# Kernel optimization log

Hardware: AMD Instinct MI355X
Metric: run time of the kernel (lower is better)

## Reference

```python
import jax, jax.numpy as jnp
import numpy as np

B, S, D, H = 2, 2048, 1024, 16
DH = D // H
MASKED_BIAS = -10000.0


def setup_inputs() -> dict:
    key = jax.random.key(0)
    k1, k2, k3 = jax.random.split(key, 3)
    x = jax.random.normal(k1, (B, S, D), dtype=jnp.float32)
    w_attn = jax.random.normal(k2, (D, 3 * D), dtype=jnp.float32) * 0.02
    b_attn = jnp.zeros((3 * D,), dtype=jnp.float32)
    w_proj = jax.random.normal(k3, (D, D), dtype=jnp.float32) * 0.02
    b_proj = jnp.zeros((D,), dtype=jnp.float32)
    return {"x": x, "w_attn": w_attn, "b_attn": b_attn, "w_proj": w_proj, "b_proj": b_proj}


def reference(x, w_attn, b_attn, w_proj, b_proj):
    # c_attn (Conv1D): [B,S,D] @ [D,3D] + b -> [B,S,3D]
    qkv = x @ w_attn + b_attn
    q, k, v = jnp.split(qkv, 3, axis=-1)

    def split_heads(t):  # [B,S,D] -> [B,H,S,DH]
        return t.reshape(B, S, H, DH).transpose(0, 2, 1, 3)

    q, k, v = split_heads(q), split_heads(k), split_heads(v)

    # scores: [B,H,S,S], scaled by sqrt(head_dim) (value.size(-1))
    scores = jnp.einsum('bhqd,bhkd->bhqk', q, k) / jnp.float32(np.sqrt(DH))

    # causal mask via torch.where against masked_bias (-10000.0), not -inf
    causal = jnp.tril(jnp.ones((S, S), dtype=bool))
    scores = jnp.where(causal, scores, jnp.float32(MASKED_BIAS))

    attn = jax.nn.softmax(scores, axis=-1)  # attn_pdrop = 0 -> dropout is identity
    ctx = jnp.einsum('bhqk,bhkd->bhqd', attn, v)  # [B,H,S,DH]

    # merge heads -> [B,S,D], then c_proj (resid_pdrop = 0)
    ctx = ctx.transpose(0, 2, 1, 3).reshape(B, S, D)
    out = ctx @ w_proj + b_proj
    return out
```

## Files before the change

### kernel.cpp

```cpp
#include <hip/hip_runtime.h>
#include <hip/hip_bf16.h>


#define BB 2
#define SS 2048
#define DD 1024
#define HH 16
#define DHH 64
#define MTOK (BB * SS)
#define N3D (3 * DD)

typedef __attribute__((ext_vector_type(8))) short bf16x8;
typedef __attribute__((ext_vector_type(4))) float f32x4;
typedef __attribute__((ext_vector_type(4))) short short4v;

__device__ __forceinline__ short f2bf(float f) {
  unsigned int x = __float_as_uint(f);
  unsigned int r = (x + 0x7fffu + ((x >> 16) & 1u)) >> 16;
  return (short)r;
}

__device__ __forceinline__ unsigned int cvtpk_bf16(float lo, float hi) {
  unsigned int r;
  asm("v_cvt_pk_bf16_f32 %0, %1, %2" : "=v"(r) : "v"(lo), "v"(hi));
  return r;
}

__global__ void cast_bf16_k(const float* __restrict__ in, short* __restrict__ out, int n4) {
  int i = blockIdx.x * blockDim.x + threadIdx.x;
  if (i < n4) {
    float4 v = reinterpret_cast<const float4*>(in)[i];
    short4v o;
    o[0] = f2bf(v.x); o[1] = f2bf(v.y); o[2] = f2bf(v.z); o[3] = f2bf(v.w);
    reinterpret_cast<short4v*>(out)[i] = o;
  }
}

__global__ void transpose_cast_k(const float* __restrict__ W, short* __restrict__ Wt, int K, int N) {
  __shared__ float t[32][33];
  int n0 = blockIdx.x * 32, k0 = blockIdx.y * 32;
  int tx = threadIdx.x, ty = threadIdx.y;
#pragma unroll
  for (int i = 0; i < 4; ++i)
    t[ty + 8 * i][tx] = W[(size_t)(k0 + ty + 8 * i) * N + n0 + tx];
  __syncthreads();
#pragma unroll
  for (int i = 0; i < 4; ++i)
    Wt[(size_t)(n0 + ty + 8 * i) * K + k0 + tx] = f2bf(t[tx][ty + 8 * i]);
}

__global__ void extract_vt_k(const short* __restrict__ qkv, short* __restrict__ vt) {
  __shared__ short t[32][33];
  int s0 = blockIdx.x * 32, d0 = blockIdx.y * 32;
  int bh = blockIdx.z;
  int b = bh >> 4, h = bh & 15;
  int tx = threadIdx.x, ty = threadIdx.y;
#pragma unroll
  for (int i = 0; i < 4; ++i)
    t[ty + 8 * i][tx] =
        qkv[(size_t)(b * SS + s0 + ty + 8 * i) * N3D + 2 * DD + h * DHH + d0 + tx];
  __syncthreads();
#pragma unroll
  for (int i = 0; i < 4; ++i)
    vt[(size_t)(bh * DHH + d0 + ty + 8 * i) * SS + s0 + tx] = t[tx][ty + 8 * i];
}

template <int OUTF32>
__global__ __launch_bounds__(256) void gemm128_k(const short* __restrict__ A,
                                                 const short* __restrict__ Bt,
                                                 const float* __restrict__ bias,
                                                 void* __restrict__ Cout,
                                                 int M, int N, int K) {
  __shared__ short As[128 * 64];
  __shared__ short Bs[128 * 64];
  int tid = threadIdx.x;
  int m0 = blockIdx.y * 128, n0 = blockIdx.x * 128;
  int w = tid >> 6, lane = tid & 63;
  int wr = w >> 1, wc = w & 1;
  int ln16 = lane & 15, l16 = lane >> 4;

  f32x4 acc[4][4] = {};

  int lrow0 = w * 32 + (lane >> 3);
  int blk_p = lane & 7;

  for (int k0 = 0; k0 < K; k0 += 64) {
#pragma unroll
    for (int i = 0; i < 4; ++i) {
      int row_p = lrow0 + i * 8;
      int colE = ((blk_p ^ (row_p & 7)) << 3);
      __builtin_amdgcn_global_load_lds(
          (const __attribute__((address_space(1))) unsigned int*)&A[(size_t)(m0 + row_p) * K + k0 + colE],
          (__attribute__((address_space(3))) unsigned int*)&As[(w * 4 + i) * 512],
          16, 0, 0);
      __builtin_amdgcn_global_load_lds(
          (const __attribute__((address_space(1))) unsigned int*)&Bt[(size_t)(n0 + row_p) * K + k0 + colE],
          (__attribute__((address_space(3))) unsigned int*)&Bs[(w * 4 + i) * 512],
          16, 0, 0);
    }
    __syncthreads();
#pragma unroll
    for (int kk = 0; kk < 2; ++kk) {
      bf16x8 a[4], bfr[4];
#pragma unroll
      for (int mi = 0; mi < 4; ++mi) {
        int row = wr * 64 + mi * 16 + ln16;
        int blk = (kk * 4 + l16) ^ (row & 7);
        a[mi] = *reinterpret_cast<const bf16x8*>(&As[row * 64 + blk * 8]);
      }
#pragma unroll
      for (int ni = 0; ni < 4; ++ni) {
        int row = wc * 64 + ni * 16 + ln16;
        int blk = (kk * 4 + l16) ^ (row & 7);
        bfr[ni] = *reinterpret_cast<const bf16x8*>(&Bs[row * 64 + blk * 8]);
      }
#pragma unroll
      for (int mi = 0; mi < 4; ++mi)
#pragma unroll
        for (int ni = 0; ni < 4; ++ni)
          acc[mi][ni] = __builtin_amdgcn_mfma_f32_16x16x32_bf16(a[mi], bfr[ni], acc[mi][ni], 0, 0, 0);
    }
    __syncthreads();
  }

#pragma unroll
  for (int mi = 0; mi < 4; ++mi)
#pragma unroll
    for (int ni = 0; ni < 4; ++ni)
#pragma unroll
      for (int ri = 0; ri < 4; ++ri) {
        int row = m0 + wr * 64 + mi * 16 + l16 * 4 + ri;
        int col = n0 + wc * 64 + ni * 16 + ln16;
        float v = acc[mi][ni][ri] + bias[col];
        if (OUTF32) {
          reinterpret_cast<float*>(Cout)[(size_t)row * N + col] = v;
        } else {
          if (col < DD) v *= 0.125f;
          reinterpret_cast<short*>(Cout)[(size_t)row * N + col] = f2bf(v);
        }
      }
}

#define MASKV -3.0e38f
__global__ __launch_bounds__(512) void flash_attn_k(const short* __restrict__ qkv,
                                                    const short* __restrict__ vt,
                                                    short* __restrict__ ctx) {
  __shared__ __align__(16) char smem[53248];
  short (*Ks)[64][72] = reinterpret_cast<short(*)[64][72]>(smem);
  short (*Vs)[64][72] = reinterpret_cast<short(*)[64][72]>(smem + 18432);
  short* Psr = reinterpret_cast<short*>(smem + 36864);
  float* Od = reinterpret_cast<float*>(smem);
  float* mls = reinterpret_cast<float*>(smem + 17408);

  int tid = threadIdx.x;
  int pj = blockIdx.x;
  int bh = blockIdx.y;
  int b = bh >> 4, h = bh & 15;
  int wg = tid >> 6, lane = tid & 63;
  int g = wg >> 2, wq = wg & 3;
  int ln16 = lane & 15, l16 = lane >> 4;
  int t8 = tid & 255;
  int tb = tid >> 8;
  int r0 = t8 >> 3, cc0 = (t8 & 7) << 3;
  int psq = (wg << 10) + (ln16 << 6);

  const short* kbase = qkv + (size_t)(b * SS) * N3D + DD + h * DHH;
  const short* vbase = vt + (size_t)(bh * DHH) * SS;

#pragma unroll 1
  for (int ti = 0; ti < 2; ++ti) {
    int qt = ti ? pj : 31 - pj;
    int q0 = qt * 64;

    bf16x8 qf[2];
    {
      const short* qrow = qkv + (size_t)(b * SS + q0 + wq * 16 + ln16) * N3D + h * DHH;
      qf[0] = *reinterpret_cast<const bf16x8*>(qrow + l16 * 8);
      qf[1] = *reinterpret_cast<const bf16x8*>(qrow + 32 + l16 * 8);
    }
    float m_ = -1e30f, l_ = 0.f;
    f32x4 cacc[4] = {};

    int ns = (qt + 2) >> 1;
    uint4 kr0, kr1, vr0, vr1;
    {
      int kt_s = tb <= qt ? tb : qt;
      kr0 = *reinterpret_cast<const uint4*>(kbase + (size_t)(kt_s * 64 + r0) * N3D + cc0);
      kr1 = *reinterpret_cast<const uint4*>(kbase + (size_t)(kt_s * 64 + r0 + 32) * N3D + cc0);
      vr0 = *reinterpret_cast<const uint4*>(vbase + (size_t)r0 * SS + kt_s * 64 + cc0);
      vr1 = *reinterpret_cast<const uint4*>(vbase + (size_t)(r0 + 32) * SS + kt_s * 64 + cc0);
    }

#pragma unroll 1
    for (int s = 0; s < ns; ++s) {
      *reinterpret_cast<uint4*>(&Ks[tb][r0][cc0]) = kr0;
      *reinterpret_cast<uint4*>(&Ks[tb][r0 + 32][cc0]) = kr1;
      *reinterpret_cast<uint4*>(&Vs[tb][r0][cc0]) = vr0;
      *reinterpret_cast<uint4*>(&Vs[tb][r0 + 32][cc0]) = vr1;
      __syncthreads();

      {
        int kt_n = 2 * (s + 1) + tb;
        if (kt_n > qt) kt_n = qt;
        kr0 = *reinterpret_cast<const uint4*>(kbase + (size_t)(kt_n * 64 + r0) * N3D + cc0);
        kr1 = *reinterpret_cast<const uint4*>(kbase + (size_t)(kt_n * 64 + r0 + 32) * N3D + cc0);
        vr0 = *reinterpret_cast<const uint4*>(vbase + (size_t)r0 * SS + kt_n * 64 + cc0);
        vr1 = *reinterpret_cast<const uint4*>(vbase + (size_t)(r0 + 32) * SS + kt_n * 64 + cc0);
      }

      int kt_c = 2 * s + g;
      if (kt_c <= qt) {
        f32x4 sacc[4] = {};
#pragma unroll
        for (int kk = 0; kk < 2; ++kk)
#pragma unroll
          for (int ni = 0; ni < 4; ++ni) {
            bf16x8 kf = *reinterpret_cast<const bf16x8*>(&Ks[g][ni * 16 + ln16][kk * 32 + l16 * 8]);
            sacc[ni] = __builtin_amdgcn_mfma_f32_16x16x32_bf16(kf, qf[kk], sacc[ni], 0, 0, 0);
          }

        float p[4][4];
        float mx = MASKV;
        if (kt_c == qt) {
          int qg = q0 + wq * 16 + ln16;
#pragma unroll
          for (int ni = 0; ni < 4; ++ni)
#pragma unroll
            for (int ri = 0; ri < 4; ++ri) {
              int kg = kt_c * 64 + ni * 16 + l16 * 4 + ri;
              float v = (kg > qg) ? MASKV : sacc[ni][ri];
              p[ni][ri] = v;
              mx = fmaxf(mx, v);
            }
        } else {
#pragma unroll
          for (int ni = 0; ni < 4; ++ni)
#pragma unroll
            for (int ri = 0; ri < 4; ++ri) {
              p[ni][ri] = sacc[ni][ri];
              mx = fmaxf(mx, sacc[ni][ri]);
            }
        }
        mx = fmaxf(mx, __shfl_xor(mx, 16));
        mx = fmaxf(mx, __shfl_xor(mx, 32));

        int keep = __all(mx <= m_ + 8.0f);
        float mn = m_;
        if (!keep) {
          mn = fmaxf(m_, mx);
          float sc = __expf(m_ - mn);
          l_ *= sc;
          float scr[4];
#pragma unroll
          for (int ri = 0; ri < 4; ++ri) scr[ri] = __shfl(sc, l16 * 4 + ri);
#pragma unroll
          for (int di = 0; di < 4; ++di)
#pragma unroll
            for (int ri = 0; ri < 4; ++ri) cacc[di][ri] *= scr[ri];
          m_ = mn;
        }

        float sum = 0.f;
#pragma unroll
        for (int ni = 0; ni < 4; ++ni)
#pragma unroll
          for (int ri = 0; ri < 4; ++ri) {
            float e = __expf(p[ni][ri] - mn);
            p[ni][ri] = e;
            sum += e;
          }
        sum += __shfl_xor(sum, 16);
        sum += __shfl_xor(sum, 32);
        l_ += sum;

#pragma unroll
        for (int ni = 0; ni < 4; ++ni) {
          uint2 u;
          u.x = cvtpk_bf16(p[ni][0], p[ni][1]);
          u.y = cvtpk_bf16(p[ni][2], p[ni][3]);
          int idx = psq + ((((ni << 1) + (l16 >> 1)) ^ (ln16 & 7)) << 3) + ((l16 & 1) << 2);
          *reinterpret_cast<uint2*>(&Psr[idx]) = u;
        }
        asm volatile("s_waitcnt lgkmcnt(0)" ::: "memory");

#pragma unroll
        for (int kk = 0; kk < 2; ++kk) {
          bf16x8 pa = *reinterpret_cast<const bf16x8*>(
              &Psr[psq + ((((kk << 2) + l16) ^ (ln16 & 7)) << 3)]);
#pragma unroll
          for (int di = 0; di < 4; ++di) {
            bf16x8 vb = *reinterpret_cast<const bf16x8*>(&Vs[g][di * 16 + ln16][kk * 32 + l16 * 8]);
            cacc[di] = __builtin_amdgcn_mfma_f32_16x16x32_bf16(pa, vb, cacc[di], 0, 0, 0);
          }
        }
      }
      __syncthreads();
    }

    if (g == 1) {
      if (l16 == 0) { mls[wq * 16 + ln16] = m_; mls[64 + wq * 16 + ln16] = l_; }
#pragma unroll
      for (int di = 0; di < 4; ++di)
#pragma unroll
        for (int ri = 0; ri < 4; ++ri)
          Od[wq * 1040 + (l16 * 4 + ri) * 65 + di * 16 + ln16] = cacc[di][ri];
    }
    __syncthreads();
    if (g == 0) {
      float m1 = mls[wq * 16 + ln16], l1 = mls[64 + wq * 16 + ln16];
      float mM = fmaxf(m_, m1);
      float e0 = __expf(m_ - mM), e1 = __expf(m1 - mM);
      float inv = 1.f / (l_ * e0 + l1 * e1);
      float e0r[4], e1r[4], ivr[4];
#pragma unroll
      for (int ri = 0; ri < 4; ++ri) {
        int src = l16 * 4 + ri;
        e0r[ri] = __shfl(e0, src);
        e1r[ri] = __shfl(e1, src);
        ivr[ri] = __shfl(inv, src);
      }
#pragma unroll
      for (int di = 0; di < 4; ++di)
#pragma unroll
        for (int ri = 0; ri < 4; ++ri) {
          float a1 = Od[wq * 1040 + (l16 * 4 + ri) * 65 + di * 16 + ln16];
          float o = (cacc[di][ri] * e0r[ri] + a1 * e1r[ri]) * ivr[ri];
          int row = q0 + wq * 16 + l16 * 4 + ri;
          int col = h * DHH + di * 16 + ln16;
          ctx[(size_t)(b * SS + row) * DD + col] = f2bf(o);
        }
    }
    __syncthreads();
  }
}

extern "C" void kernel_launch(void* const* d_in, const int* in_sizes, int n_in,
                              void* d_out, int out_size, void* d_ws, size_t ws_size,
                              hipStream_t stream) {
  const float* x      = (const float*)d_in[0];
  const float* w_attn = (const float*)d_in[1];
  const float* b_attn = (const float*)d_in[2];
  const float* w_proj = (const float*)d_in[3];
  const float* b_proj = (const float*)d_in[4];
  float* out = (float*)d_out;

  char* ws = (char*)d_ws;
  short* xb     = (short*)(ws);
  short* wattnT = (short*)(ws + 8388608);
  short* wprojT = (short*)(ws + 14680064);
  short* qkv    = (short*)(ws + 16777216);
  short* vt     = (short*)(ws + 41943040);
  short* ctx    = (short*)(ws + 50331648);

  {
    int n4 = (MTOK * DD) / 4;
    cast_bf16_k<<<(n4 + 255) / 256, 256, 0, stream>>>(x, xb, n4);
  }
  transpose_cast_k<<<dim3(N3D / 32, DD / 32), dim3(32, 8), 0, stream>>>(w_attn, wattnT, DD, N3D);
  transpose_cast_k<<<dim3(DD / 32, DD / 32), dim3(32, 8), 0, stream>>>(w_proj, wprojT, DD, DD);
  gemm128_k<0><<<dim3(N3D / 128, MTOK / 128), 256, 0, stream>>>(xb, wattnT, b_attn, qkv, MTOK, N3D, DD);
  extract_vt_k<<<dim3(SS / 32, DHH / 32, BB * HH), dim3(32, 8), 0, stream>>>(qkv, vt);
  flash_attn_k<<<dim3(16, BB * HH), 512, 0, stream>>>(qkv, vt, ctx);
  gemm128_k<1><<<dim3(DD / 128, MTOK / 128), 256, 0, stream>>>(ctx, wprojT, b_proj, out, MTOK, DD, DD);
}
```

Measured before the change: 127.3 us.

## Launch one query tile per block and XOR-swizzle K/V shared memory

Result: slower. 144.7 us (+13.6%).

```diff
diff --git a/kernel.cpp b/kernel.cpp
--- a/kernel.cpp
+++ b/kernel.cpp
@@ -145,192 +145,189 @@
 __global__ __launch_bounds__(512) void flash_attn_k(const short* __restrict__ qkv,
                                                     const short* __restrict__ vt,
                                                     short* __restrict__ ctx) {
-  __shared__ __align__(16) char smem[53248];
-  short (*Ks)[64][72] = reinterpret_cast<short(*)[64][72]>(smem);
-  short (*Vs)[64][72] = reinterpret_cast<short(*)[64][72]>(smem + 18432);
-  short* Psr = reinterpret_cast<short*>(smem + 36864);
+  __shared__ __align__(16) char smem[49152];
+  short* Sm = reinterpret_cast<short*>(smem);
   float* Od = reinterpret_cast<float*>(smem);
   float* mls = reinterpret_cast<float*>(smem + 17408);
 
   int tid = threadIdx.x;
-  int pj = blockIdx.x;
+  int qt = 31 - blockIdx.x;
   int bh = blockIdx.y;
   int b = bh >> 4, h = bh & 15;
+  int q0 = qt * 64;
   int wg = tid >> 6, lane = tid & 63;
   int g = wg >> 2, wq = wg & 3;
   int ln16 = lane & 15, l16 = lane >> 4;
   int t8 = tid & 255;
   int tb = tid >> 8;
-  int r0 = t8 >> 3, cc0 = (t8 & 7) << 3;
-  int psq = (wg << 10) + (ln16 << 6);
+  int r0 = t8 >> 3, cb = t8 & 7;
+  int ksw = tb * 4096 + r0 * 64 + ((cb ^ (r0 & 7)) << 3);
+  int psq = 16384 + (wg << 10) + (ln16 << 6);
 
   const short* kbase = qkv + (size_t)(b * SS) * N3D + DD + h * DHH;
   const short* vbase = vt + (size_t)(bh * DHH) * SS;
 
+  bf16x8 qf[2];
+  {
+    const short* qrow = qkv + (size_t)(b * SS + q0 + wq * 16 + ln16) * N3D + h * DHH;
+    qf[0] = *reinterpret_cast<const bf16x8*>(qrow + l16 * 8);
+    qf[1] = *reinterpret_cast<const bf16x8*>(qrow + 32 + l16 * 8);
+  }
+  float m_ = -1e30f, l_ = 0.f;
+  f32x4 cacc[4] = {};
+
+  int ns = (qt + 2) >> 1;
+  uint4 kr0, kr1, vr0, vr1;
+  {
+    int kt_s = tb <= qt ? tb : qt;
+    kr0 = *reinterpret_cast<const uint4*>(kbase + (size_t)(kt_s * 64 + r0) * N3D + cb * 8);
+    kr1 = *reinterpret_cast<const uint4*>(kbase + (size_t)(kt_s * 64 + r0 + 32) * N3D + cb * 8);
+    vr0 = *reinterpret_cast<const uint4*>(vbase + (size_t)r0 * SS + kt_s * 64 + cb * 8);
+    vr1 = *reinterpret_cast<const uint4*>(vbase + (size_t)(r0 + 32) * SS + kt_s * 64 + cb * 8);
+  }
+
 #pragma unroll 1
-  for (int ti = 0; ti < 2; ++ti) {
-    int qt = ti ? pj : 31 - pj;
-    int q0 = qt * 64;
-
-    bf16x8 qf[2];
+  for (int s = 0; s < ns; ++s) {
+    *reinterpret_cast<uint4*>(&Sm[ksw]) = kr0;
+    *reinterpret_cast<uint4*>(&Sm[ksw + 2048]) = kr1;
+    *reinterpret_cast<uint4*>(&Sm[8192 + ksw]) = vr0;
+    *reinterpret_cast<uint4*>(&Sm[8192 + ksw + 2048]) = vr1;
+    __syncthreads();
+
     {
-      const short* qrow = qkv + (size_t)(b * SS + q0 + wq * 16 + ln16) * N3D + h * DHH;
-      qf[0] = *reinterpret_cast<const bf16x8*>(qrow + l16 * 8);
-      qf[1] = *reinterpret_cast<const bf16x8*>(qrow + 32 + l16 * 8);
-    }
-    float m_ = -1e30f, l_ = 0.f;
-    f32x4 cacc[4] = {};
-
-    int ns = (qt + 2) >> 1;
-    uint4 kr0, kr1, vr0, vr1;
-    {
-      int kt_s = tb <= qt ? tb : qt;
-      kr0 = *reinterpret_cast<const uint4*>(kbase + (size_t)(kt_s * 64 + r0) * N3D + cc0);
-      kr1 = *reinterpret_cast<const uint4*>(kbase + (size_t)(kt_s * 64 + r0 + 32) * N3D + cc0);
-      vr0 = *reinterpret_cast<const uint4*>(vbase + (size_t)r0 * SS + kt_s * 64 + cc0);
-      vr1 = *reinterpret_cast<const uint4*>(vbase + (size_t)(r0 + 32) * SS + kt_s * 64 + cc0);
-    }
-
-#pragma unroll 1
-    for (int s = 0; s < ns; ++s) {
-      *reinterpret_cast<uint4*>(&Ks[tb][r0][cc0]) = kr0;
-      *reinterpret_cast<uint4*>(&Ks[tb][r0 + 32][cc0]) = kr1;
-      *reinterpret_cast<uint4*>(&Vs[tb][r0][cc0]) = vr0;
-      *reinterpret_cast<uint4*>(&Vs[tb][r0 + 32][cc0]) = vr1;
-      __syncthreads();
-
-      {
-        int kt_n = 2 * (s + 1) + tb;
-        if (kt_n > qt) kt_n = qt;
-        kr0 = *reinterpret_cast<const uint4*>(kbase + (size_t)(kt_n * 64 + r0) * N3D + cc0);
-        kr1 = *reinterpret_cast<const uint4*>(kbase + (size_t)(kt_n * 64 + r0 + 32) * N3D + cc0);
-        vr0 = *reinterpret_cast<const uint4*>(vbase + (size_t)r0 * SS + kt_n * 64 + cc0);
-        vr1 = *reinterpret_cast<const uint4*>(vbase + (size_t)(r0 + 32) * SS + kt_n * 64 + cc0);
-      }
-
-      int kt_c = 2 * s + g;
-      if (kt_c <= qt) {
-        f32x4 sacc[4] = {};
-#pragma unroll
-        for (int kk = 0; kk < 2; ++kk)
-#pragma unroll
-          for (int ni = 0; ni < 4; ++ni) {
-            bf16x8 kf = *reinterpret_cast<const bf16x8*>(&Ks[g][ni * 16 + ln16][kk * 32 + l16 * 8]);
-            sacc[ni] = __builtin_amdgcn_mfma_f32_16x16x32_bf16(kf, qf[kk], sacc[ni], 0, 0, 0);
+      int kt_n = 2 * (s + 1) + tb;
+      if (kt_n > qt) kt_n = qt;
+      kr0 = *reinterpret_cast<const uint4*>(kbase + (size_t)(kt_n * 64 + r0) * N3D + cb * 8);
+      kr1 = *reinterpret_cast<const uint4*>(kbase + (size_t)(kt_n * 64 + r0 + 32) * N3D + cb * 8);
+      vr0 = *reinterpret_cast<const uint4*>(vbase + (size_t)r0 * SS + kt_n * 64 + cb * 8);
+      vr1 = *reinterpret_cast<const uint4*>(vbase + (size_t)(r0 + 32) * SS + kt_n * 64 + cb * 8);
+    }
+
+    int kt_c = 2 * s + g;
+    if (kt_c <= qt) {
+      f32x4 sacc[4] = {};
+#pragma unroll
+      for (int kk = 0; kk < 2; ++kk)
+#pragma unroll
+        for (int ni = 0; ni < 4; ++ni) {
+          int row = ni * 16 + ln16;
+          bf16x8 kf = *reinterpret_cast<const bf16x8*>(
+              &Sm[g * 4096 + row * 64 + (((kk * 4 + l16) ^ (row & 7)) << 3)]);
+          sacc[ni] = __builtin_amdgcn_mfma_f32_16x16x32_bf16(kf, qf[kk], sacc[ni], 0, 0, 0);
+        }
+
+      float p[4][4];
+      float mx = MASKV;
+      if (kt_c == qt) {
+        int qg = q0 + wq * 16 + ln16;
+#pragma unroll
+        for (int ni = 0; ni < 4; ++ni)
+#pragma unroll
+          for (int ri = 0; ri < 4; ++ri) {
+            int kg = kt_c * 64 + ni * 16 + l16 * 4 + ri;
+            float v = (kg > qg) ? MASKV : sacc[ni][ri];
+            p[ni][ri] = v;
+            mx = fmaxf(mx, v);
           }
-
-        float p[4][4];
-        float mx = MASKV;
-        if (kt_c == qt) {
-          int qg = q0 + wq * 16 + ln16;
-#pragma unroll
-          for (int ni = 0; ni < 4; ++ni)
-#pragma unroll
-            for (int ri = 0; ri < 4; ++ri) {
-              int kg = kt_c * 64 + ni * 16 + l16 * 4 + ri;
-              float v = (kg > qg) ? MASKV : sacc[ni][ri];
-              p[ni][ri] = v;
-              mx = fmaxf(mx, v);
-            }
-        } else {
-#pragma unroll
-          for (int ni = 0; ni < 4; ++ni)
-#pragma unroll
-            for (int ri = 0; ri < 4; ++ri) {
-              p[ni][ri] = sacc[ni][ri];
-              mx = fmaxf(mx, sacc[ni][ri]);
-            }
+      } else {
+#pragma unroll
+        for (int ni = 0; ni < 4; ++ni)
+#pragma unroll
+          for (int ri = 0; ri < 4; ++ri) {
+            p[ni][ri] = sacc[ni][ri];
+            mx = fmaxf(mx, sacc[ni][ri]);
+          }
+      }
+      mx = fmaxf(mx, __shfl_xor(mx, 16));
+      mx = fmaxf(mx, __shfl_xor(mx, 32));
+
+      int keep = __all(mx <= m_ + 8.0f);
+      float mn = m_;
+      if (!keep) {
+        mn = fmaxf(m_, mx);
+        float sc = __expf(m_ - mn);
+        l_ *= sc;
+        float scr[4];
+#pragma unroll
+        for (int ri = 0; ri < 4; ++ri) scr[ri] = __shfl(sc, l16 * 4 + ri);
+#pragma unroll
+        for (int di = 0; di < 4; ++di)
+#pragma unroll
+          for (int ri = 0; ri < 4; ++ri) cacc[di][ri] *= scr[ri];
+        m_ = mn;
+      }
+
+      float sum = 0.f;
+#pragma unroll
+      for (int ni = 0; ni < 4; ++ni)
+#pragma unroll
+        for (int ri = 0; ri < 4; ++ri) {
+          float e = __expf(p[ni][ri] - mn);
+          p[ni][ri] = e;
+          sum += e;
         }
-        mx = fmaxf(mx, __shfl_xor(mx, 16));
-        mx = fmaxf(mx, __shfl_xor(mx, 32));
-
-        int keep = __all(mx <= m_ + 8.0f);
-        float mn = m_;
-        if (!keep) {
-          mn = fmaxf(m_, mx);
-          float sc = __expf(m_ - mn);
-          l_ *= sc;
-          float scr[4];
-#pragma unroll
-          for (int ri = 0; ri < 4; ++ri) scr[ri] = __shfl(sc, l16 * 4 + ri);
-#pragma unroll
-          for (int di = 0; di < 4; ++di)
-#pragma unroll
-            for (int ri = 0; ri < 4; ++ri) cacc[di][ri] *= scr[ri];
-          m_ = mn;
+      sum += __shfl_xor(sum, 16);
+      sum += __shfl_xor(sum, 32);
+      l_ += sum;
+
+#pragma unroll
+      for (int ni = 0; ni < 4; ++ni) {
+        uint2 u;
+        u.x = cvtpk_bf16(p[ni][0], p[ni][1]);
+        u.y = cvtpk_bf16(p[ni][2], p[ni][3]);
+        int idx = psq + ((((ni << 1) + (l16 >> 1)) ^ (ln16 & 7)) << 3) + ((l16 & 1) << 2);
+        *reinterpret_cast<uint2*>(&Sm[idx]) = u;
+      }
+      asm volatile("s_waitcnt lgkmcnt(0)" ::: "memory");
+
+#pragma unroll
+      for (int kk = 0; kk < 2; ++kk) {
+        bf16x8 pa = *reinterpret_cast<const bf16x8*>(
+            &Sm[psq + ((((kk << 2) + l16) ^ (ln16 & 7)) << 3)]);
+#pragma unroll
+        for (int di = 0; di < 4; ++di) {
+          int row = di * 16 + ln16;
+          bf16x8 vb = *reinterpret_cast<const bf16x8*>(
+              &Sm[8192 + g * 4096 + row * 64 + (((kk * 4 + l16) ^ (row & 7)) << 3)]);
+          cacc[di] = __builtin_amdgcn_mfma_f32_16x16x32_bf16(pa, vb, cacc[di], 0, 0, 0);
         }
-
-        float sum = 0.f;
-#pragma unroll
-        for (int ni = 0; ni < 4; ++ni)
-#pragma unroll
-          for (int ri = 0; ri < 4; ++ri) {
-            float e = __expf(p[ni][ri] - mn);
-            p[ni][ri] = e;
-            sum += e;
-          }
-        sum += __shfl_xor(sum, 16);
-        sum += __shfl_xor(sum, 32);
-        l_ += sum;
-
-#pragma unroll
-        for (int ni = 0; ni < 4; ++ni) {
-          uint2 u;
-          u.x = cvtpk_bf16(p[ni][0], p[ni][1]);
-          u.y = cvtpk_bf16(p[ni][2], p[ni][3]);
-          int idx = psq + ((((ni << 1) + (l16 >> 1)) ^ (ln16 & 7)) << 3) + ((l16 & 1) << 2);
-          *reinterpret_cast<uint2*>(&Psr[idx]) = u;
-        }
-        asm volatile("s_waitcnt lgkmcnt(0)" ::: "memory");
-
-#pragma unroll
-        for (int kk = 0; kk < 2; ++kk) {
-          bf16x8 pa = *reinterpret_cast<const bf16x8*>(
-              &Psr[psq + ((((kk << 2) + l16) ^ (ln16 & 7)) << 3)]);
-#pragma unroll
-          for (int di = 0; di < 4; ++di) {
-            bf16x8 vb = *reinterpret_cast<const bf16x8*>(&Vs[g][di * 16 + ln16][kk * 32 + l16 * 8]);
-            cacc[di] = __builtin_amdgcn_mfma_f32_16x16x32_bf16(pa, vb, cacc[di], 0, 0, 0);
-          }
-        }
-      }
-      __syncthreads();
-    }
-
-    if (g == 1) {
-      if (l16 == 0) { mls[wq * 16 + ln16] = m_; mls[64 + wq * 16 + ln16] = l_; }
-#pragma unroll
-      for (int di = 0; di < 4; ++di)
-#pragma unroll
-        for (int ri = 0; ri < 4; ++ri)
-          Od[wq * 1040 + (l16 * 4 + ri) * 65 + di * 16 + ln16] = cacc[di][ri];
+      }
     }
     __syncthreads();
-    if (g == 0) {
-      float m1 = mls[wq * 16 + ln16], l1 = mls[64 + wq * 16 + ln16];
-      float mM = fmaxf(m_, m1);
-      float e0 = __expf(m_ - mM), e1 = __expf(m1 - mM);
-      float inv = 1.f / (l_ * e0 + l1 * e1);
-      float e0r[4], e1r[4], ivr[4];
+  }
+
+  if (g == 1) {
+    if (l16 == 0) { mls[wq * 16 + ln16] = m_; mls[64 + wq * 16 + ln16] = l_; }
+#pragma unroll
+    for (int di = 0; di < 4; ++di)
+#pragma unroll
+      for (int ri = 0; ri < 4; ++ri)
+        Od[wq * 1040 + (l16 * 4 + ri) * 65 + di * 16 + ln16] = cacc[di][ri];
+  }
+  __syncthreads();
+  if (g == 0) {
+    float m1 = mls[wq * 16 + ln16], l1 = mls[64 + wq * 16 + ln16];
+    float mM = fmaxf(m_, m1);
+    float e0 = __expf(m_ - mM), e1 = __expf(m1 - mM);
+    float inv = 1.f / (l_ * e0 + l1 * e1);
+    float e0r[4], e1r[4], ivr[4];
+#pragma unroll
+    for (int ri = 0; ri < 4; ++ri) {
+      int src = l16 * 4 + ri;
+      e0r[ri] = __shfl(e0, src);
+      e1r[ri] = __shfl(e1, src);
+      ivr[ri] = __shfl(inv, src);
+    }
+#pragma unroll
+    for (int di = 0; di < 4; ++di)
 #pragma unroll
       for (int ri = 0; ri < 4; ++ri) {
-        int src = l16 * 4 + ri;
-        e0r[ri] = __shfl(e0, src);
-        e1r[ri] = __shfl(e1, src);
-        ivr[ri] = __shfl(inv, src);
-      }
-#pragma unroll
-      for (int di = 0; di < 4; ++di)
-#pragma unroll
-        for (int ri = 0; ri < 4; ++ri) {
-          float a1 = Od[wq * 1040 + (l16 * 4 + ri) * 65 + di * 16 + ln16];
-          float o = (cacc[di][ri] * e0r[ri] + a1 * e1r[ri]) * ivr[ri];
-          int row = q0 + wq * 16 + l16 * 4 + ri;
-          int col = h * DHH + di * 16 + ln16;
-          ctx[(size_t)(b * SS + row) * DD + col] = f2bf(o);
-        }
-    }
-    __syncthreads();
+        float a1 = Od[wq * 1040 + (l16 * 4 + ri) * 65 + di * 16 + ln16];
+        float o = (cacc[di][ri] * e0r[ri] + a1 * e1r[ri]) * ivr[ri];
+        int row = q0 + wq * 16 + l16 * 4 + ri;
+        int col = h * DHH + di * 16 + ln16;
+        ctx[(size_t)(b * SS + row) * DD + col] = f2bf(o);
+      }
   }
 }
 
@@ -360,6 +357,6 @@
   transpose_cast_k<<<dim3(DD / 32, DD / 32), dim3(32, 8), 0, stream>>>(w_proj, wprojT, DD, DD);
   gemm128_k<0><<<dim3(N3D / 128, MTOK / 128), 256, 0, stream>>>(xb, wattnT, b_attn, qkv, MTOK, N3D, DD);
   extract_vt_k<<<dim3(SS / 32, DHH / 32, BB * HH), dim3(32, 8), 0, stream>>>(qkv, vt);
-  flash_attn_k<<<dim3(16, BB * HH), 512, 0, stream>>>(qkv, vt, ctx);
+  flash_attn_k<<<dim3(32, BB * HH), 512, 0, stream>>>(qkv, vt, ctx);
   gemm128_k<1><<<dim3(DD / 128, MTOK / 128), 256, 0, stream>>>(ctx, wprojT, b_proj, out, MTOK, DD, DD);
 }
```

## Fuse V-transpose into QKV GEMM epilogue and switch softmax to exp2

Applied to the files above, without the earlier changes.

After: 128.4 us. Within noise of the previous version (+0.8%).

```diff
diff --git a/kernel.cpp b/kernel.cpp
--- a/kernel.cpp
+++ b/kernel.cpp
@@ -9,6 +9,7 @@
 #define DHH 64
 #define MTOK (BB * SS)
 #define N3D (3 * DD)
+#define QSCALE 0.18033688f
 
 typedef __attribute__((ext_vector_type(8))) short bf16x8;
 typedef __attribute__((ext_vector_type(4))) float f32x4;
@@ -49,27 +50,12 @@
     Wt[(size_t)(n0 + ty + 8 * i) * K + k0 + tx] = f2bf(t[tx][ty + 8 * i]);
 }
 
-__global__ void extract_vt_k(const short* __restrict__ qkv, short* __restrict__ vt) {
-  __shared__ short t[32][33];
-  int s0 = blockIdx.x * 32, d0 = blockIdx.y * 32;
-  int bh = blockIdx.z;
-  int b = bh >> 4, h = bh & 15;
-  int tx = threadIdx.x, ty = threadIdx.y;
-#pragma unroll
-  for (int i = 0; i < 4; ++i)
-    t[ty + 8 * i][tx] =
-        qkv[(size_t)(b * SS + s0 + ty + 8 * i) * N3D + 2 * DD + h * DHH + d0 + tx];
-  __syncthreads();
-#pragma unroll
-  for (int i = 0; i < 4; ++i)
-    vt[(size_t)(bh * DHH + d0 + ty + 8 * i) * SS + s0 + tx] = t[tx][ty + 8 * i];
-}
-
 template <int OUTF32>
 __global__ __launch_bounds__(256) void gemm128_k(const short* __restrict__ A,
                                                  const short* __restrict__ Bt,
                                                  const float* __restrict__ bias,
                                                  void* __restrict__ Cout,
+                                                 short* __restrict__ vtout,
                                                  int M, int N, int K) {
   __shared__ short As[128 * 64];
   __shared__ short Bs[128 * 64];
@@ -135,8 +121,14 @@
         if (OUTF32) {
           reinterpret_cast<float*>(Cout)[(size_t)row * N + col] = v;
         } else {
-          if (col < DD) v *= 0.125f;
-          reinterpret_cast<short*>(Cout)[(size_t)row * N + col] = f2bf(v);
+          if (n0 < DD) v *= QSCALE;
+          short bv = f2bf(v);
+          if (n0 >= 2 * DD) {
+            int bb = row >> 11, s = row & 2047;
+            vtout[(size_t)(bb * 1024 + col - 2 * DD) * SS + s] = bv;
+          } else {
+            reinterpret_cast<short*>(Cout)[(size_t)row * N + col] = bv;
+          }
         }
       }
 }
@@ -244,11 +236,11 @@
         mx = fmaxf(mx, __shfl_xor(mx, 16));
         mx = fmaxf(mx, __shfl_xor(mx, 32));
 
-        int keep = __all(mx <= m_ + 8.0f);
+        int keep = __all(mx <= m_ + 11.5f);
         float mn = m_;
         if (!keep) {
           mn = fmaxf(m_, mx);
-          float sc = __expf(m_ - mn);
+          float sc = exp2f(m_ - mn);
           l_ *= sc;
           float scr[4];
 #pragma unroll
@@ -265,7 +257,7 @@
         for (int ni = 0; ni < 4; ++ni)
 #pragma unroll
           for (int ri = 0; ri < 4; ++ri) {
-            float e = __expf(p[ni][ri] - mn);
+            float e = exp2f(p[ni][ri] - mn);
             p[ni][ri] = e;
             sum += e;
           }
@@ -309,7 +301,7 @@
     if (g == 0) {
       float m1 = mls[wq * 16 + ln16], l1 = mls[64 + wq * 16 + ln16];
       float mM = fmaxf(m_, m1);
-      float e0 = __expf(m_ - mM), e1 = __expf(m1 - mM);
+      float e0 = exp2f(m_ - mM), e1 = exp2f(m1 - mM);
       float inv = 1.f / (l_ * e0 + l1 * e1);
       float e0r[4], e1r[4], ivr[4];
 #pragma unroll
@@ -358,8 +350,7 @@
   }
   transpose_cast_k<<<dim3(N3D / 32, DD / 32), dim3(32, 8), 0, stream>>>(w_attn, wattnT, DD, N3D);
   transpose_cast_k<<<dim3(DD / 32, DD / 32), dim3(32, 8), 0, stream>>>(w_proj, wprojT, DD, DD);
-  gemm128_k<0><<<dim3(N3D / 128, MTOK / 128), 256, 0, stream>>>(xb, wattnT, b_attn, qkv, MTOK, N3D, DD);
-  extract_vt_k<<<dim3(SS / 32, DHH / 32, BB * HH), dim3(32, 8), 0, stream>>>(qkv, vt);
+  gemm128_k<0><<<dim3(N3D / 128, MTOK / 128), 256, 0, stream>>>(xb, wattnT, b_attn, qkv, vt, MTOK, N3D, DD);
   flash_attn_k<<<dim3(16, BB * HH), 512, 0, stream>>>(qkv, vt, ctx);
-  gemm128_k<1><<<dim3(DD / 128, MTOK / 128), 256, 0, stream>>>(ctx, wprojT, b_proj, out, MTOK, DD, DD);
-}
+  gemm128_k<1><<<dim3(DD / 128, MTOK / 128), 256, 0, stream>>>(ctx, wprojT, b_proj, out, nullptr, MTOK, DD, DD);
+}
```
